# Performance work log

Measured on AMD Instinct MI355X. Metric: run time of the kernel, lower is better.

## Reference

```python
import jax, jax.numpy as jnp
import numpy as np

BINS = 32  # bins_num


def setup_inputs() -> dict:
    key = jax.random.key(0)
    imgs_in = jax.random.uniform(key, (64, 3, 512, 512), dtype=jnp.float32)
    return {"imgs_in": imgs_in}


def _multiscale_hist(x):
    # x: [b, c, h, w] with h, w even -> F.interpolate to (h//2*2, w//2*2, 'area')
    # is an exact identity, so tgt_imgs == x.
    b, c, h, w = x.shape
    hh, ww = h // 2, w // 2

    # torch.histc(bins=BINS, min=0, max=1): values outside [0,1] ignored,
    # value == 1 lands in the last bin.
    bin_idx = jnp.clip(jnp.floor(x * BINS).astype(jnp.int32), 0, BINS - 1)
    valid = ((x >= 0.0) & (x <= 1.0)).astype(x.dtype)

    # Split image into 2x2 quadrants (the scale-1 tiles); scale-0 histogram
    # over the full image is the sum of the 4 quadrant counts.
    bin_q = bin_idx.reshape(b, c, 2, hh, 2, ww)
    val_q = valid.reshape(b, c, 2, hh, 2, ww)
    region = (jnp.arange(b).reshape(b, 1, 1, 1, 1, 1) * 4
              + jnp.arange(2).reshape(1, 1, 2, 1, 1, 1) * 2
              + jnp.arange(2).reshape(1, 1, 1, 1, 2, 1))
    flat = (region * BINS + bin_q).ravel()

    counts = jax.ops.segment_sum(val_q.ravel(), flat,
                                 num_segments=b * 4 * BINS)
    counts = counts.reshape(b, 2, 2, BINS)  # per-quadrant counts

    s1 = counts / jnp.asarray(hh * ww, x.dtype)          # [b, 2, 2, BINS]
    s0 = counts.sum(axis=(1, 2)) / jnp.asarray(h * w, x.dtype)  # [b, BINS]

    # Scale 0: one histogram broadcast over the full 4x4 grid.
    h0 = jnp.broadcast_to(s0[:, :, None, None], (b, BINS, 4, 4))
    # Scale 1: each quadrant histogram fills its 2x2 block of the 4x4 grid.
    h1 = s1.transpose(0, 3, 1, 2)                         # [b, BINS, 2, 2]
    h1 = jnp.repeat(jnp.repeat(h1, 2, axis=2), 2, axis=3)  # [b, BINS, 4, 4]
    # Third bins_num block is never written (num_scales == 2) -> zeros.
    h2 = jnp.zeros((b, BINS, 4, 4), x.dtype)
    return jnp.concatenate([h0, h1, h2], axis=1)  # [b, 3*BINS, 4, 4]


def reference(imgs_in) -> jnp.ndarray:
    return _multiscale_hist(imgs_in)
```

## Files before the change

kernel.cpp:

```cpp
#include <hip/hip_runtime.h>

#define BINS   32
#define NB     64
#define NCH    3
#define HH     512
#define WW     512
#define SLICES 8

typedef float vfloat4 __attribute__((ext_vector_type(4)));


__global__ __launch_bounds__(256, 8) void hist_main(const float* __restrict__ in,
                                                    unsigned* __restrict__ counts) {
    __shared__ unsigned whist[8][BINS];

    const int t    = threadIdx.x;
    const int bid  = blockIdx.x;
    const int s    = bid & (SLICES - 1);
    const int quad = (bid >> 3) & 3;
    const int b    = bid >> 5;
    const int qr   = quad >> 1;
    const int qc   = quad & 1;
    const int sub  = t >> 5;

    whist[t >> 5][t & 31] = 0;
    __syncthreads();

    const size_t base = (size_t)b * (NCH * HH * WW)
                      + (size_t)qr * (256 * WW)
                      + (size_t)qc * 256;

    #pragma unroll 2
    for (int it = 0; it < 24; ++it) {
        const int f    = it * 256 + t;
        const int Rrel = f >> 6;
        const int col4 = f & 63;
        const int R    = s * 96 + Rrel;
        const int c    = R >> 8;
        const int r    = R & 255;
        const vfloat4* p = (const vfloat4*)(in + base
                                            + (size_t)c * (HH * WW)
                                            + (size_t)r * WW
                                            + (size_t)col4 * 4);
        const vfloat4 v = __builtin_nontemporal_load(p);
        #pragma unroll
        for (int u = 0; u < 4; ++u) {
            int bin = (int)(v[u] * 32.0f);
            bin = bin < 0 ? 0 : (bin > 31 ? 31 : bin);
            atomicAdd(&whist[sub][bin], 1u);
        }
    }
    __syncthreads();

    if (t < 32) {
        unsigned tot = 0;
        #pragma unroll
        for (int g = 0; g < 8; ++g) tot += whist[g][t];
        atomicAdd(&counts[(b * 4 + quad) * BINS + t], tot);
    }
}

__global__ __launch_bounds__(256) void finalize(const unsigned* __restrict__ counts,
                                                float* __restrict__ out, int n) {
    const int idx = blockIdx.x * 256 + threadIdx.x;
    if (idx >= n) return;
    const int j  = idx & 3;
    const int i  = (idx >> 2) & 3;
    const int ch = (idx >> 4) % 96;
    const int b  = idx / 1536;
    float val = 0.0f;
    if (ch < 32) {
        const unsigned ssum = counts[(b * 4 + 0) * BINS + ch]
                            + counts[(b * 4 + 1) * BINS + ch]
                            + counts[(b * 4 + 2) * BINS + ch]
                            + counts[(b * 4 + 3) * BINS + ch];
        val = (float)ssum * (1.0f / 262144.0f);
    } else if (ch < 64) {
        const int bin = ch - 32;
        const int q   = (i >> 1) * 2 + (j >> 1);
        val = (float)counts[(b * 4 + q) * BINS + bin] * (1.0f / 65536.0f);
    }
    out[idx] = val;
}

extern "C" void kernel_launch(void* const* d_in, const int* in_sizes, int n_in,
                              void* d_out, int out_size, void* d_ws, size_t ws_size,
                              hipStream_t stream) {
    const float* in = (const float*)d_in[0];
    float* out      = (float*)d_out;
    unsigned* counts = (unsigned*)d_ws;

    (void)hipMemsetAsync(counts, 0, NB * 4 * BINS * sizeof(unsigned), stream);
    hist_main<<<NB * 4 * SLICES, 256, 0, stream>>>(in, counts);
    finalize<<<(out_size + 255) / 256, 256, 0, stream>>>(counts, out, out_size);
}
```

Baseline: 254.1 us.

## Privatize shared histogram per lane pair with packed 16-bit counters, drop global atomics

Each pair of threads now gets its own column of the shared histogram, laid out [4][32 bins][32 lanes]. The two threads in a pair share one 32-bit word, each adding into a separate 16-bit half. This removes the contention between threads of a wavefront that previously hit the same bin with LDS atomics. Each block writes its per-slice partial counts to workspace without atomics, which also removes the memset. The finalize kernel then sums over the slices. The cost is a larger LDS footprint (16KB per block, which can limit occupancy) and a more expensive in-block reduction.

```diff
diff --git a/kernel.cpp b/kernel.cpp
--- a/kernel.cpp
+++ b/kernel.cpp
@@ -11,8 +11,8 @@
 
 
 __global__ __launch_bounds__(256, 8) void hist_main(const float* __restrict__ in,
-                                                    unsigned* __restrict__ counts) {
-    __shared__ unsigned whist[8][BINS];
+                                                    unsigned* __restrict__ scounts) {
+    __shared__ unsigned whist[4][BINS][32];
 
     const int t    = threadIdx.x;
     const int bid  = blockIdx.x;
@@ -21,10 +21,13 @@
     const int b    = bid >> 5;
     const int qr   = quad >> 1;
     const int qc   = quad & 1;
-    const int sub  = t >> 5;
 
-    whist[t >> 5][t & 31] = 0;
+    #pragma unroll
+    for (int k = 0; k < 16; ++k) ((unsigned*)whist)[k * 256 + t] = 0;
     __syncthreads();
+
+    const unsigned inc = 1u << ((t & 1) << 4);
+    unsigned* const hp = &whist[t >> 6][0][(t >> 1) & 31];
 
     const size_t base = (size_t)b * (NCH * HH * WW)
                       + (size_t)qr * (256 * WW)
@@ -47,20 +50,32 @@
         for (int u = 0; u < 4; ++u) {
             int bin = (int)(v[u] * 32.0f);
             bin = bin < 0 ? 0 : (bin > 31 ? 31 : bin);
-            atomicAdd(&whist[sub][bin], 1u);
+            atomicAdd(hp + (bin << 5), inc);
         }
     }
     __syncthreads();
 
-    if (t < 32) {
-        unsigned tot = 0;
+    {
+        const int bin = t >> 3;
+        const int src = t & 7;
+        const int w   = src & 3;
+        const int hf  = src >> 2;
+        unsigned part = 0;
         #pragma unroll
-        for (int g = 0; g < 8; ++g) tot += whist[g][t];
-        atomicAdd(&counts[(b * 4 + quad) * BINS + t], tot);
+        for (int i = 0; i < 16; ++i) {
+            const int p = hf * 16 + ((i + bin) & 15);
+            const unsigned word = whist[w][bin][p];
+            part += (word & 0xffffu) + (word >> 16);
+        }
+        part += __shfl_xor(part, 1);
+        part += __shfl_xor(part, 2);
+        part += __shfl_xor(part, 4);
+        if (src == 0)
+            scounts[(((b * 4 + quad) * SLICES) + s) * BINS + bin] = part;
     }
 }
 
-__global__ __launch_bounds__(256) void finalize(const unsigned* __restrict__ counts,
+__global__ __launch_bounds__(256) void finalize(const unsigned* __restrict__ scounts,
                                                 float* __restrict__ out, int n) {
     const int idx = blockIdx.x * 256 + threadIdx.x;
     if (idx >= n) return;
@@ -70,15 +85,21 @@
     const int b  = idx / 1536;
     float val = 0.0f;
     if (ch < 32) {
-        const unsigned ssum = counts[(b * 4 + 0) * BINS + ch]
-                            + counts[(b * 4 + 1) * BINS + ch]
-                            + counts[(b * 4 + 2) * BINS + ch]
-                            + counts[(b * 4 + 3) * BINS + ch];
+        unsigned ssum = 0;
+        #pragma unroll
+        for (int q = 0; q < 4; ++q)
+            #pragma unroll
+            for (int sl = 0; sl < SLICES; ++sl)
+                ssum += scounts[(((b * 4 + q) * SLICES) + sl) * BINS + ch];
         val = (float)ssum * (1.0f / 262144.0f);
     } else if (ch < 64) {
         const int bin = ch - 32;
         const int q   = (i >> 1) * 2 + (j >> 1);
-        val = (float)counts[(b * 4 + q) * BINS + bin] * (1.0f / 65536.0f);
+        unsigned ssum = 0;
+        #pragma unroll
+        for (int sl = 0; sl < SLICES; ++sl)
+            ssum += scounts[(((b * 4 + q) * SLICES) + sl) * BINS + bin];
+        val = (float)ssum * (1.0f / 65536.0f);
     }
     out[idx] = val;
 }
@@ -88,9 +109,8 @@
                               hipStream_t stream) {
     const float* in = (const float*)d_in[0];
     float* out      = (float*)d_out;
-    unsigned* counts = (unsigned*)d_ws;
+    unsigned* scounts = (unsigned*)d_ws;
 
-    (void)hipMemsetAsync(counts, 0, NB * 4 * BINS * sizeof(unsigned), stream);
-    hist_main<<<NB * 4 * SLICES, 256, 0, stream>>>(in, counts);
-    finalize<<<(out_size + 255) / 256, 256, 0, stream>>>(counts, out, out_size);
+    hist_main<<<NB * 4 * SLICES, 256, 0, stream>>>(in, scounts);
+    finalize<<<(out_size + 255) / 256, 256, 0, stream>>>(scounts, out, out_size);
 }
```

Measured after the change: 254.1 us. Within noise of the previous version (-0.0%).
